# Kernel optimization log

Measured on AMD Instinct MI355X. Metric: run time of the kernel, lower is better.

## Reference

```python
import jax, jax.numpy as jnp
import numpy as np

B, GL, GF, N = 4, 4, 128, 1024
CS, CN, NA = 32, 16, 16
S, HS = 512, 512


def squash(s, axis):
    # mag_sq/(1+mag_sq) * s/mag == s * mag/(1+mag_sq)
    mag_sq = jnp.sum(s * s, axis=axis, keepdims=True)
    return s * (jnp.sqrt(mag_sq) / (1.0 + mag_sq))


def routing(u_hat, n_iter=3):
    # u_hat: [M, I, J, U]; dynamic routing, softmax over J, squash over J (as in source)
    M, I, J, U = u_hat.shape
    b = jnp.zeros((I, J), dtype=u_hat.dtype)
    v = None
    for _ in range(n_iter):
        c = jax.nn.softmax(b, axis=1)                       # [I, J]
        s = jnp.einsum('ij,miju->mju', c, u_hat)            # [M, J, U]
        v = squash(s, axis=1)                               # squash over J (torch dim=2)
        b = b + jnp.einsum('miju,mju->mij', u_hat, v).mean(axis=0)
    return v


def setup_inputs():
    key = jax.random.key(0)
    ks = jax.random.split(key, 7)
    sc = 0.1
    return {
        'graph_embed': jax.random.normal(ks[0], (B, GL, GF, N), jnp.float32),
        'hidden': jax.random.normal(ks[1], (B, S, HS), jnp.float32),
        'Wp': jax.random.normal(ks[2], (GL, CS, GL, GF), jnp.float32) * sc,  # per-unit conv kernels
        'bp': jax.random.normal(ks[3], (GL, CS), jnp.float32) * sc,
        'Wg': jax.random.normal(ks[4], (CS, CN, CS, GL), jnp.float32) * sc,  # graph caps [I,J,U,K]
        'Wa': jax.random.normal(ks[5], (CS + HS,), jnp.float32) * sc,        # attention_1 weight
        'Ws': jax.random.normal(ks[6], (CN, NA, CS, CS), jnp.float32) * sc,  # aspect caps [I,J,U,K]
    }


def _per_example(x, h, Wp, bp, Wg, Wa, Ws):
    # x: [GL, GF, N], h: [S, HS]
    gl, gf, n = x.shape
    # primary capsules: each unit's conv kernel covers all (GL,GF) -> full contraction
    u = jnp.einsum('uclf,lfn->ucn', Wp, x) + bp[:, :, None]   # [GL, CS, N]
    u = squash(u.reshape(gl, -1), axis=1)                     # squash over CS*N (torch dim=2)
    p = u.reshape(n, gl, CS)                                  # torch .view(-1, GL, CS)
    # graph capsule routing
    u_hat_g = jnp.einsum('ijuk,mik->miju', Wg, p.transpose(0, 2, 1))  # [N, CS, CN, CS]
    v_g = routing(u_hat_g)                                    # [N, CN, CS]
    g = v_g.reshape(n, CS, CN).mean(axis=0).reshape(CN, CS)   # torch .view semantics
    # adaptive attention: Linear([g;h]) with no bias, softmax over capsules
    score = jax.nn.softmax((g @ Wa[:CS])[None, :] + (h @ Wa[CS:])[:, None], axis=1)  # [S, CN]
    condensed = g[None, :, :] * score[:, :, None]             # [S, CN, CS]
    # aspect capsule routing (transpose(1,2) then layer-internal transpose cancel out)
    u_hat_a = jnp.einsum('ijuk,mik->miju', Ws, condensed)     # [S, CN, NA, CS]
    return routing(u_hat_a)                                   # [S, NA, CS]


def reference(graph_embed, hidden, Wp, bp, Wg, Wa, Ws):
    f = jax.vmap(_per_example, in_axes=(0, 0, None, None, None, None, None))
    return f(graph_embed, hidden, Wp, bp, Wg, Wa, Ws)   # [B, S, NA, CS]
```

## Files before the change

### kernel.cpp

```cpp
#include <hip/hip_runtime.h>
#include <math.h>


static constexpr int OFF_U  = 0;
static constexpr int OFF_S  = 524288;
static constexpr int OFF_SS = 2621440;
static constexpr int OFF_BG = 2621456;
static constexpr int OFF_G  = 2623504;
static constexpr int OFF_VA = 2625552;
static constexpr int OFF_MS = 2627600;
static constexpr int OFF_UH = 2758672;

__global__ void k_primary_part(const float* __restrict__ X, const float* __restrict__ Wp,
                               float* __restrict__ Upart)
{
    __shared__ float Wt[128 * 68];
    const int ct = blockIdx.x, nt = blockIdx.y;
    const int b = blockIdx.z >> 2, ks = blockIdx.z & 3;
    const int t = threadIdx.x;
    const int tn = t & 15, tc = t >> 4;
    const int c0 = ct * 64, n0 = nt * 64;
#pragma unroll
    for (int i = 0; i < 8; ++i) {
        const int idx = t + i * 256;
        const int c = idx >> 5, k4 = idx & 31;
        const float4 wv = *(const float4*)&Wp[(size_t)(c0 + c) * 512 + ks * 128 + k4 * 4];
        Wt[(k4 * 4 + 0) * 68 + c] = wv.x;
        Wt[(k4 * 4 + 1) * 68 + c] = wv.y;
        Wt[(k4 * 4 + 2) * 68 + c] = wv.z;
        Wt[(k4 * 4 + 3) * 68 + c] = wv.w;
    }
    __syncthreads();
    float acc[4][4] = {};
    const float* Xp = X + (size_t)b * 524288 + (size_t)(ks * 128) * 1024 + n0 + tn * 4;
#pragma unroll 4
    for (int k = 0; k < 128; ++k) {
        const float4 xv = *(const float4*)(Xp + (size_t)k * 1024);
        const float4 wv = *(const float4*)&Wt[k * 68 + tc * 4];
        const float w[4] = {wv.x, wv.y, wv.z, wv.w};
        const float x[4] = {xv.x, xv.y, xv.z, xv.w};
#pragma unroll
        for (int ci = 0; ci < 4; ++ci)
#pragma unroll
            for (int ni = 0; ni < 4; ++ni)
                acc[ci][ni] = fmaf(w[ci], x[ni], acc[ci][ni]);
    }
    float* up = Upart + (size_t)ks * 524288 + (size_t)b * 131072;
#pragma unroll
    for (int ci = 0; ci < 4; ++ci)
        *(float4*)&up[(size_t)(c0 + tc * 4 + ci) * 1024 + n0 + tn * 4] =
            make_float4(acc[ci][0], acc[ci][1], acc[ci][2], acc[ci][3]);
}

__global__ void k_reduceU(const float* __restrict__ Upart, const float* __restrict__ bp,
                          float* __restrict__ U, float* __restrict__ SS)
{
    __shared__ float red[256];
    const int blk = blockIdx.x, t = threadIdx.x;
    const int b = blk >> 5, cg = blk & 31;
    float ssq = 0.f;
#pragma unroll
    for (int i = 0; i < 4; ++i) {
        const int c = cg * 4 + i;
        const int f4 = b * 32768 + c * 256 + t;
        float4 s = ((const float4*)Upart)[f4];
#pragma unroll
        for (int ks = 1; ks < 4; ++ks) {
            const float4 p = ((const float4*)Upart)[ks * 131072 + f4];
            s.x += p.x; s.y += p.y; s.z += p.z; s.w += p.w;
        }
        const float bv = bp[c];
        s.x += bv; s.y += bv; s.z += bv; s.w += bv;
        ssq = fmaf(s.x, s.x, ssq); ssq = fmaf(s.y, s.y, ssq);
        ssq = fmaf(s.z, s.z, ssq); ssq = fmaf(s.w, s.w, ssq);
        ((float4*)U)[f4] = s;
    }
    red[t] = ssq;
    __syncthreads();
    for (int s = 128; s > 0; s >>= 1) {
        if (t < s) red[t] += red[t + s];
        __syncthreads();
    }
    if (t == 0) atomicAdd(&SS[b * 4 + (cg >> 3)], red[0]);
}

__global__ void k_smatmul(const float* __restrict__ U, const float* __restrict__ SS,
                          const float* __restrict__ Bg, const float* __restrict__ Wg,
                          float* __restrict__ S)
{
    __shared__ float Pt[64 * 65];
    __shared__ float Ct[64 * 65];
    __shared__ float cls[512];
    const int mt = blockIdx.x, jt = blockIdx.y, b = blockIdx.z;
    const int t = threadIdx.x;
    const int tj = t & 15, tm = t >> 4;
    if (t < 32) {
        float vals[16];
        float mx = -1e30f;
        for (int j = 0; j < 16; ++j) { vals[j] = Bg[b * 512 + t * 16 + j]; mx = fmaxf(mx, vals[j]); }
        float sum = 0.f;
        for (int j = 0; j < 16; ++j) { vals[j] = expf(vals[j] - mx); sum += vals[j]; }
        const float inv = 1.f / sum;
        for (int j = 0; j < 16; ++j) cls[t * 16 + j] = vals[j] * inv;
    }
    const float ss = SS[b * 4 + (mt >> 2)];
    const float sc = sqrtf(ss) / (1.f + ss);
    float acc[4][4] = {};
    const float* Ub = U + (size_t)b * 131072 + (size_t)mt * 64 * 128;
    __syncthreads();
    for (int kc = 0; kc < 2; ++kc) {
        for (int x = t; x < 64 * 64; x += 256) {
            const int r = x >> 6, cq = x & 63;
            Pt[r * 65 + cq] = Ub[r * 128 + kc * 64 + cq] * sc;
            const int q = kc * 64 + cq;
            const int i = q & 31, kk = q >> 5;
            const int ju = jt * 64 + r;
            const int j = ju >> 5, u = ju & 31;
            Ct[r * 65 + cq] = cls[i * 16 + j] * Wg[((i * 16 + j) * 32 + u) * 4 + kk];
        }
        __syncthreads();
        for (int q = 0; q < 64; ++q) {
            float pv[4], cv[4];
#pragma unroll
            for (int mm = 0; mm < 4; ++mm) pv[mm] = Pt[(tm * 4 + mm) * 65 + q];
#pragma unroll
            for (int jj = 0; jj < 4; ++jj) cv[jj] = Ct[(tj * 4 + jj) * 65 + q];
#pragma unroll
            for (int mm = 0; mm < 4; ++mm)
#pragma unroll
                for (int jj = 0; jj < 4; ++jj)
                    acc[mm][jj] = fmaf(pv[mm], cv[jj], acc[mm][jj]);
        }
        __syncthreads();
    }
#pragma unroll
    for (int mm = 0; mm < 4; ++mm) {
        float4 w = make_float4(acc[mm][0], acc[mm][1], acc[mm][2], acc[mm][3]);
        *(float4*)(S + (size_t)b * 524288 + (size_t)(mt * 64 + tm * 4 + mm) * 512
                     + jt * 64 + tj * 4) = w;
    }
}

__global__ void k_mag(const float* __restrict__ S, float* __restrict__ MS)
{
    const int t = threadIdx.x;
    const int u = t & 31, ml = t >> 5;
    const int m = blockIdx.x * 8 + ml;
    const int b = blockIdx.y;
    const float* row = S + (size_t)b * 524288 + (size_t)m * 512;
    float mag = 0.f;
#pragma unroll
    for (int j = 0; j < 16; ++j) { const float v = row[j * 32 + u]; mag = fmaf(v, v, mag); }
    MS[b * 32768 + m * 32 + u] = sqrtf(mag) / (1.f + mag);
}

__global__ void k_maggmean(const float* __restrict__ S, float* __restrict__ G)
{
    __shared__ float gacc[512];
    const int t = threadIdx.x;
    gacc[t] = 0.f; gacc[t + 256] = 0.f;
    const int u = t & 31, mlg = t >> 5;
    const int b = blockIdx.y;
    const int m0 = blockIdx.x * 32 + mlg * 4;
    float preg[16];
#pragma unroll
    for (int j = 0; j < 16; ++j) preg[j] = 0.f;
    __syncthreads();
#pragma unroll
    for (int mi = 0; mi < 4; ++mi) {
        const float* row = S + (size_t)b * 524288 + (size_t)(m0 + mi) * 512;
        float sv[16];
        float mag = 0.f;
#pragma unroll
        for (int j = 0; j < 16; ++j) { sv[j] = row[j * 32 + u]; mag = fmaf(sv[j], sv[j], mag); }
        const float msc = sqrtf(mag) / (1.f + mag);
#pragma unroll
        for (int j = 0; j < 16; ++j) preg[j] = fmaf(sv[j], msc, preg[j]);
    }
#pragma unroll
    for (int j = 0; j < 16; ++j) atomicAdd(&gacc[j * 32 + u], preg[j]);
    __syncthreads();
    atomicAdd(&G[b * 512 + t], gacc[t] * (1.f / 1024.f));
    atomicAdd(&G[b * 512 + 256 + t], gacc[t + 256] * (1.f / 1024.f));
}

__global__ void k_tbu(const float* __restrict__ U, const float* __restrict__ SS,
                      const float* __restrict__ S, const float* __restrict__ MS,
                      const float* __restrict__ Wg, float* __restrict__ Bg)
{
    __shared__ float Ps[64 * 132];
    __shared__ float Vs[64 * 68];
    __shared__ float bup[64];
    const int jt = blockIdx.x, mc = blockIdx.y, b = blockIdx.z;
    const int t = threadIdx.x;
    const int tq = t & 31, tjv = t >> 5;
    const int m0 = mc * 64;
    if (t < 64) bup[t] = 0.f;
    const float ss = SS[b * 4 + (mc >> 2)];
    const float sc = sqrtf(ss) / (1.f + ss);
#pragma unroll
    for (int i = 0; i < 8; ++i) {
        const int f4 = t + i * 256;
        const int r = f4 >> 5, q4 = f4 & 31;
        float4 v = *(const float4*)&U[(size_t)b * 131072 + (size_t)(m0 + r) * 128 + q4 * 4];
        v.x *= sc; v.y *= sc; v.z *= sc; v.w *= sc;
        *(float4*)&Ps[r * 132 + q4 * 4] = v;
    }
#pragma unroll
    for (int i = 0; i < 4; ++i) {
        const int f4 = t + i * 256;
        const int r = f4 >> 4, c4 = f4 & 15;
        const int m = m0 + r;
        float4 v = *(const float4*)&S[(size_t)b * 524288 + (size_t)m * 512 + jt * 64 + c4 * 4];
        const int ub = (c4 * 4) & 31;
        const float* msp = MS + b * 32768 + m * 32;
        v.x *= msp[ub + 0]; v.y *= msp[ub + 1]; v.z *= msp[ub + 2]; v.w *= msp[ub + 3];
        *(float4*)&Vs[r * 68 + c4 * 4] = v;
    }
    __syncthreads();
    float acc[4][8] = {};
#pragma unroll 2
    for (int m = 0; m < 64; ++m) {
        const float4 p4 = *(const float4*)&Ps[m * 132 + tq * 4];
        const float4 va = *(const float4*)&Vs[m * 68 + tjv * 8];
        const float4 vb = *(const float4*)&Vs[m * 68 + tjv * 8 + 4];
        const float pv[4] = {p4.x, p4.y, p4.z, p4.w};
        const float vv[8] = {va.x, va.y, va.z, va.w, vb.x, vb.y, vb.z, vb.w};
#pragma unroll
        for (int qi = 0; qi < 4; ++qi)
#pragma unroll
            for (int ji = 0; ji < 8; ++ji)
                acc[qi][ji] = fmaf(pv[qi], vv[ji], acc[qi][ji]);
    }
    const int k = tq >> 3;
    const int j_loc = tjv >> 2;
    const int j = jt * 2 + j_loc;
    const int u0 = (tjv & 3) * 8;
#pragma unroll
    for (int qi = 0; qi < 4; ++qi) {
        const int i = (tq & 7) * 4 + qi;
        const float* wp = Wg + ((i * 16 + j) * 32) * 4 + k;
        float s = 0.f;
#pragma unroll
        for (int ji = 0; ji < 8; ++ji)
            s = fmaf(wp[(u0 + ji) * 4], acc[qi][ji], s);
        s += __shfl_xor(s, 8);
        s += __shfl_xor(s, 16);
        s += __shfl_xor(s, 32);
        if ((t & 56) == 0) atomicAdd(&bup[i * 2 + j_loc], s);
    }
    __syncthreads();
    if (t < 64) {
        const int ii = t >> 1, jl = t & 1;
        atomicAdd(&Bg[b * 512 + ii * 16 + jt * 2 + jl], bup[t] * (1.f / 1024.f));
    }
}

__global__ void k_uhat(const float* __restrict__ G, const float* __restrict__ Wa,
                       const float* __restrict__ Ws, float* __restrict__ UH)
{
    const int b = blockIdx.y;
    const int t = threadIdx.x;
    __shared__ float g[512], cond[512], score[16], red[16];
    g[t] = G[b * 512 + t];
    g[t + 256] = G[b * 512 + 256 + t];
    __syncthreads();
    if (t < 16) {
        float s = 0.f;
        for (int u = 0; u < 32; ++u) s = fmaf(g[t * 32 + u], Wa[u], s);
        red[t] = s;
    }
    __syncthreads();
    if (t == 0) {
        float mx = -1e30f;
        for (int j = 0; j < 16; ++j) mx = fmaxf(mx, red[j]);
        float sum = 0.f;
        for (int j = 0; j < 16; ++j) { score[j] = expf(red[j] - mx); sum += score[j]; }
        const float inv = 1.f / sum;
        for (int j = 0; j < 16; ++j) score[j] *= inv;
    }
    __syncthreads();
    cond[t] = g[t] * score[t >> 5];
    cond[t + 256] = g[t + 256] * score[(t + 256) >> 5];
    __syncthreads();
    const int e0 = blockIdx.x * 1024 + t * 4;
    const int i = e0 >> 9;
    const float* cp = cond + i * 32;
    const float* wp = Ws + (size_t)e0 * 32;
    float res[4];
#pragma unroll
    for (int jj = 0; jj < 4; ++jj) {
        float s = 0.f;
#pragma unroll
        for (int k8 = 0; k8 < 8; ++k8) {
            const float4 w = *(const float4*)(wp + jj * 32 + k8 * 4);
            s = fmaf(w.x, cp[k8 * 4 + 0], s);
            s = fmaf(w.y, cp[k8 * 4 + 1], s);
            s = fmaf(w.z, cp[k8 * 4 + 2], s);
            s = fmaf(w.w, cp[k8 * 4 + 3], s);
        }
        res[jj] = s;
    }
    ((float4*)UH)[(b * 8192 + e0) >> 2] = make_float4(res[0], res[1], res[2], res[3]);
}

__global__ void k_route(const float* __restrict__ UH, float* __restrict__ VA)
{
    const int b = blockIdx.x;
    const int t = threadIdx.x;
    __shared__ float uh[8192], ba[256], cc[256], sbuf[512], msc[32];
#pragma unroll
    for (int i = 0; i < 8; ++i)
        ((float4*)uh)[i * 256 + t] = ((const float4*)UH)[b * 2048 + i * 256 + t];
    ba[t] = 0.f;
    __syncthreads();
    for (int it = 0; it < 3; ++it) {
        if (t < 16) {
            float mx = -1e30f;
            for (int j = 0; j < 16; ++j) mx = fmaxf(mx, ba[t * 16 + j]);
            float sum = 0.f;
            for (int j = 0; j < 16; ++j) { cc[t * 16 + j] = expf(ba[t * 16 + j] - mx); sum += cc[t * 16 + j]; }
            const float inv = 1.f / sum;
            for (int j = 0; j < 16; ++j) cc[t * 16 + j] *= inv;
        }
        __syncthreads();
        for (int h = 0; h < 2; ++h) {
            const int e = h * 256 + t;
            const int j = e >> 5;
            float s = 0.f;
            for (int i = 0; i < 16; ++i) s = fmaf(cc[i * 16 + j], uh[i * 512 + e], s);
            sbuf[e] = s;
        }
        __syncthreads();
        if (t < 32) {
            float mg = 0.f;
            for (int j = 0; j < 16; ++j) { const float x = sbuf[j * 32 + t]; mg = fmaf(x, x, mg); }
            msc[t] = sqrtf(mg) / (1.f + mg);
        }
        __syncthreads();
        for (int h = 0; h < 2; ++h) {
            const int e = h * 256 + t;
            sbuf[e] *= msc[e & 31];
        }
        __syncthreads();
        if (it < 2) {
            const int i = t >> 4, j = t & 15;
            float s = 0.f;
            for (int u = 0; u < 32; ++u) s = fmaf(uh[i * 512 + j * 32 + u], sbuf[j * 32 + u], s);
            ba[t] += s;
            __syncthreads();
        }
    }
    VA[b * 512 + t] = sbuf[t];
    VA[b * 512 + 256 + t] = sbuf[256 + t];
}

__global__ void k_out(const float* __restrict__ VA, float* __restrict__ out)
{
    const int idx = blockIdx.x * 256 + threadIdx.x;
    const int b = idx >> 16;
    const int jv4 = idx & 127;
    ((float4*)out)[idx] = ((const float4*)VA)[b * 128 + jv4];
}

extern "C" void kernel_launch(void* const* d_in, const int* in_sizes, int n_in,
                              void* d_out, int out_size, void* d_ws, size_t ws_size,
                              hipStream_t stream)
{
    const float* X   = (const float*)d_in[0];
    const float* Wp  = (const float*)d_in[2];
    const float* bp  = (const float*)d_in[3];
    const float* Wg  = (const float*)d_in[4];
    const float* Wa  = (const float*)d_in[5];
    const float* Wsp = (const float*)d_in[6];
    float* out = (float*)d_out;
    float* ws = (float*)d_ws;

    float* U  = ws + OFF_U;
    float* S  = ws + OFF_S;
    float* SS = ws + OFF_SS;
    float* Bg = ws + OFF_BG;
    float* G  = ws + OFF_G;
    float* VA = ws + OFF_VA;
    float* MS = ws + OFF_MS;
    float* UH = ws + OFF_UH;

    hipMemsetAsync(SS, 0, (16 + 2048 + 2048) * sizeof(float), stream);

    k_primary_part<<<dim3(2, 16, 16), 256, 0, stream>>>(X, Wp, S);
    k_reduceU<<<128, 256, 0, stream>>>(S, bp, U, SS);

    for (int it = 0; it < 3; ++it) {
        k_smatmul<<<dim3(16, 8, 4), 256, 0, stream>>>(U, SS, Bg, Wg, S);
        if (it < 2) {
            k_mag<<<dim3(128, 4), 256, 0, stream>>>(S, MS);
            k_tbu<<<dim3(8, 16, 4), 256, 0, stream>>>(U, SS, S, MS, Wg, Bg);
        } else {
            k_maggmean<<<dim3(32, 4), 256, 0, stream>>>(S, G);
        }
    }

    k_uhat<<<dim3(8, 4), 256, 0, stream>>>(G, Wa, Wsp, UH);
    k_route<<<4, 256, 0, stream>>>(UH, VA);
    k_out<<<1024, 256, 0, stream>>>(VA, out);
}
```

Before: 230.1 us.

## Fold memset, magnitude and output-broadcast kernels into neighbouring kernels

Removes the memset by zeroing the accumulators inside the first kernel, fuses the per-row squash-magnitude computation into the agreement kernel via shared memory, and merges routing with the output broadcast. The aim is to cut kernel launch count and the MS global buffer. In exchange, magnitudes are recomputed redundantly by each column-tile block and routing is redone in every output block.

```diff
diff --git a/kernel.cpp b/kernel.cpp
--- a/kernel.cpp
+++ b/kernel.cpp
@@ -7,14 +7,17 @@
 static constexpr int OFF_SS = 2621440;
 static constexpr int OFF_BG = 2621456;
 static constexpr int OFF_G  = 2623504;
-static constexpr int OFF_VA = 2625552;
-static constexpr int OFF_MS = 2627600;
-static constexpr int OFF_UH = 2758672;
+static constexpr int OFF_UH = 2625552;
 
 __global__ void k_primary_part(const float* __restrict__ X, const float* __restrict__ Wp,
-                               float* __restrict__ Upart)
+                               float* __restrict__ ws)
 {
     __shared__ float Wt[128 * 68];
+    float* Upart = ws + OFF_S;
+    if (blockIdx.x == 0 && blockIdx.y == 0 && blockIdx.z == 0) {
+        float* Z = ws + OFF_SS;
+        for (int i = threadIdx.x; i < 4112; i += 256) Z[i] = 0.f;
+    }
     const int ct = blockIdx.x, nt = blockIdx.y;
     const int b = blockIdx.z >> 2, ks = blockIdx.z & 3;
     const int t = threadIdx.x;
@@ -52,10 +55,12 @@
             make_float4(acc[ci][0], acc[ci][1], acc[ci][2], acc[ci][3]);
 }
 
-__global__ void k_reduceU(const float* __restrict__ Upart, const float* __restrict__ bp,
-                          float* __restrict__ U, float* __restrict__ SS)
+__global__ void k_reduceU(const float* __restrict__ bp, float* __restrict__ ws)
 {
     __shared__ float red[256];
+    const float* Upart = ws + OFF_S;
+    float* U  = ws + OFF_U;
+    float* SS = ws + OFF_SS;
     const int blk = blockIdx.x, t = threadIdx.x;
     const int b = blk >> 5, cg = blk & 31;
     float ssq = 0.f;
@@ -84,13 +89,15 @@
     if (t == 0) atomicAdd(&SS[b * 4 + (cg >> 3)], red[0]);
 }
 
-__global__ void k_smatmul(const float* __restrict__ U, const float* __restrict__ SS,
-                          const float* __restrict__ Bg, const float* __restrict__ Wg,
-                          float* __restrict__ S)
+__global__ void k_smatmul(const float* __restrict__ Wg, float* __restrict__ ws)
 {
     __shared__ float Pt[64 * 65];
     __shared__ float Ct[64 * 65];
     __shared__ float cls[512];
+    const float* U  = ws + OFF_U;
+    const float* SS = ws + OFF_SS;
+    const float* Bg = ws + OFF_BG;
+    float* S = ws + OFF_S;
     const int mt = blockIdx.x, jt = blockIdx.y, b = blockIdx.z;
     const int t = threadIdx.x;
     const int tj = t & 15, tm = t >> 4;
@@ -103,8 +110,8 @@
         const float inv = 1.f / sum;
         for (int j = 0; j < 16; ++j) cls[t * 16 + j] = vals[j] * inv;
     }
-    const float ss = SS[b * 4 + (mt >> 2)];
-    const float sc = sqrtf(ss) / (1.f + ss);
+    const float ssv = SS[b * 4 + (mt >> 2)];
+    const float sc = sqrtf(ssv) / (1.f + ssv);
     float acc[4][4] = {};
     const float* Ub = U + (size_t)b * 131072 + (size_t)mt * 64 * 128;
     __syncthreads();
@@ -115,8 +122,8 @@
             const int q = kc * 64 + cq;
             const int i = q & 31, kk = q >> 5;
             const int ju = jt * 64 + r;
-            const int j = ju >> 5, u = ju & 31;
-            Ct[r * 65 + cq] = cls[i * 16 + j] * Wg[((i * 16 + j) * 32 + u) * 4 + kk];
+            const int j = ju >> 5, uu = ju & 31;
+            Ct[r * 65 + cq] = cls[i * 16 + j] * Wg[((i * 16 + j) * 32 + uu) * 4 + kk];
         }
         __syncthreads();
         for (int q = 0; q < 64; ++q) {
@@ -141,63 +148,36 @@
     }
 }
 
-__global__ void k_mag(const float* __restrict__ S, float* __restrict__ MS)
-{
-    const int t = threadIdx.x;
-    const int u = t & 31, ml = t >> 5;
-    const int m = blockIdx.x * 8 + ml;
-    const int b = blockIdx.y;
-    const float* row = S + (size_t)b * 524288 + (size_t)m * 512;
-    float mag = 0.f;
-#pragma unroll
-    for (int j = 0; j < 16; ++j) { const float v = row[j * 32 + u]; mag = fmaf(v, v, mag); }
-    MS[b * 32768 + m * 32 + u] = sqrtf(mag) / (1.f + mag);
-}
-
-__global__ void k_maggmean(const float* __restrict__ S, float* __restrict__ G)
-{
-    __shared__ float gacc[512];
-    const int t = threadIdx.x;
-    gacc[t] = 0.f; gacc[t + 256] = 0.f;
-    const int u = t & 31, mlg = t >> 5;
-    const int b = blockIdx.y;
-    const int m0 = blockIdx.x * 32 + mlg * 4;
-    float preg[16];
-#pragma unroll
-    for (int j = 0; j < 16; ++j) preg[j] = 0.f;
-    __syncthreads();
-#pragma unroll
-    for (int mi = 0; mi < 4; ++mi) {
-        const float* row = S + (size_t)b * 524288 + (size_t)(m0 + mi) * 512;
-        float sv[16];
-        float mag = 0.f;
-#pragma unroll
-        for (int j = 0; j < 16; ++j) { sv[j] = row[j * 32 + u]; mag = fmaf(sv[j], sv[j], mag); }
-        const float msc = sqrtf(mag) / (1.f + mag);
-#pragma unroll
-        for (int j = 0; j < 16; ++j) preg[j] = fmaf(sv[j], msc, preg[j]);
-    }
-#pragma unroll
-    for (int j = 0; j < 16; ++j) atomicAdd(&gacc[j * 32 + u], preg[j]);
-    __syncthreads();
-    atomicAdd(&G[b * 512 + t], gacc[t] * (1.f / 1024.f));
-    atomicAdd(&G[b * 512 + 256 + t], gacc[t + 256] * (1.f / 1024.f));
-}
-
-__global__ void k_tbu(const float* __restrict__ U, const float* __restrict__ SS,
-                      const float* __restrict__ S, const float* __restrict__ MS,
-                      const float* __restrict__ Wg, float* __restrict__ Bg)
+__global__ void k_tbu(const float* __restrict__ Wg, float* __restrict__ ws)
 {
     __shared__ float Ps[64 * 132];
     __shared__ float Vs[64 * 68];
+    __shared__ float msS[64 * 32];
     __shared__ float bup[64];
+    const float* U  = ws + OFF_U;
+    const float* SS = ws + OFF_SS;
+    const float* S  = ws + OFF_S;
+    float* Bg = ws + OFF_BG;
     const int jt = blockIdx.x, mc = blockIdx.y, b = blockIdx.z;
     const int t = threadIdx.x;
     const int tq = t & 31, tjv = t >> 5;
     const int m0 = mc * 64;
     if (t < 64) bup[t] = 0.f;
-    const float ss = SS[b * 4 + (mc >> 2)];
-    const float sc = sqrtf(ss) / (1.f + ss);
+    {
+        const int uu = t & 31, rg = t >> 5;
+#pragma unroll
+        for (int mi = 0; mi < 8; ++mi) {
+            const int r = rg * 8 + mi;
+            const float* row = S + (size_t)b * 524288 + (size_t)(m0 + r) * 512;
+            float mag = 0.f;
+#pragma unroll
+            for (int j = 0; j < 16; ++j) { const float v = row[j * 32 + uu]; mag = fmaf(v, v, mag); }
+            msS[r * 32 + uu] = sqrtf(mag) / (1.f + mag);
+        }
+    }
+    const float ssv = SS[b * 4 + (mc >> 2)];
+    const float sc = sqrtf(ssv) / (1.f + ssv);
+    __syncthreads();
 #pragma unroll
     for (int i = 0; i < 8; ++i) {
         const int f4 = t + i * 256;
@@ -213,8 +193,8 @@
         const int m = m0 + r;
         float4 v = *(const float4*)&S[(size_t)b * 524288 + (size_t)m * 512 + jt * 64 + c4 * 4];
         const int ub = (c4 * 4) & 31;
-        const float* msp = MS + b * 32768 + m * 32;
-        v.x *= msp[ub + 0]; v.y *= msp[ub + 1]; v.z *= msp[ub + 2]; v.w *= msp[ub + 3];
+        v.x *= msS[r * 32 + ub + 0]; v.y *= msS[r * 32 + ub + 1];
+        v.z *= msS[r * 32 + ub + 2]; v.w *= msS[r * 32 + ub + 3];
         *(float4*)&Vs[r * 68 + c4 * 4] = v;
     }
     __syncthreads();
@@ -256,9 +236,43 @@
     }
 }
 
-__global__ void k_uhat(const float* __restrict__ G, const float* __restrict__ Wa,
-                       const float* __restrict__ Ws, float* __restrict__ UH)
-{
+__global__ void k_maggmean(float* __restrict__ ws)
+{
+    __shared__ float gacc[512];
+    const float* S = ws + OFF_S;
+    float* G = ws + OFF_G;
+    const int t = threadIdx.x;
+    gacc[t] = 0.f; gacc[t + 256] = 0.f;
+    const int uu = t & 31, mlg = t >> 5;
+    const int b = blockIdx.y;
+    const int m0 = blockIdx.x * 32 + mlg * 4;
+    float preg[16];
+#pragma unroll
+    for (int j = 0; j < 16; ++j) preg[j] = 0.f;
+    __syncthreads();
+#pragma unroll
+    for (int mi = 0; mi < 4; ++mi) {
+        const float* row = S + (size_t)b * 524288 + (size_t)(m0 + mi) * 512;
+        float sv[16];
+        float mag = 0.f;
+#pragma unroll
+        for (int j = 0; j < 16; ++j) { sv[j] = row[j * 32 + uu]; mag = fmaf(sv[j], sv[j], mag); }
+        const float msc = sqrtf(mag) / (1.f + mag);
+#pragma unroll
+        for (int j = 0; j < 16; ++j) preg[j] = fmaf(sv[j], msc, preg[j]);
+    }
+#pragma unroll
+    for (int j = 0; j < 16; ++j) atomicAdd(&gacc[j * 32 + uu], preg[j]);
+    __syncthreads();
+    atomicAdd(&G[b * 512 + t], gacc[t] * (1.f / 1024.f));
+    atomicAdd(&G[b * 512 + 256 + t], gacc[t + 256] * (1.f / 1024.f));
+}
+
+__global__ void k_uhat(const float* __restrict__ Wa, const float* __restrict__ Wsp,
+                       float* __restrict__ ws)
+{
+    const float* G = ws + OFF_G;
+    float* UH = ws + OFF_UH;
     const int b = blockIdx.y;
     const int t = threadIdx.x;
     __shared__ float g[512], cond[512], score[16], red[16];
@@ -267,7 +281,7 @@
     __syncthreads();
     if (t < 16) {
         float s = 0.f;
-        for (int u = 0; u < 32; ++u) s = fmaf(g[t * 32 + u], Wa[u], s);
+        for (int uu = 0; uu < 32; ++uu) s = fmaf(g[t * 32 + uu], Wa[uu], s);
         red[t] = s;
     }
     __syncthreads();
@@ -286,7 +300,7 @@
     const int e0 = blockIdx.x * 1024 + t * 4;
     const int i = e0 >> 9;
     const float* cp = cond + i * 32;
-    const float* wp = Ws + (size_t)e0 * 32;
+    const float* wp = Wsp + (size_t)e0 * 32;
     float res[4];
 #pragma unroll
     for (int jj = 0; jj < 4; ++jj) {
@@ -304,11 +318,13 @@
     ((float4*)UH)[(b * 8192 + e0) >> 2] = make_float4(res[0], res[1], res[2], res[3]);
 }
 
-__global__ void k_route(const float* __restrict__ UH, float* __restrict__ VA)
-{
-    const int b = blockIdx.x;
+__global__ void k_route_out(float* __restrict__ ws, float* __restrict__ out)
+{
+    const float* UH = ws + OFF_UH;
+    const int bid = blockIdx.x;
     const int t = threadIdx.x;
     __shared__ float uh[8192], ba[256], cc[256], sbuf[512], msc[32];
+    const int b = bid >> 6;
 #pragma unroll
     for (int i = 0; i < 8; ++i)
         ((float4*)uh)[i * 256 + t] = ((const float4*)UH)[b * 2048 + i * 256 + t];
@@ -346,21 +362,17 @@
         if (it < 2) {
             const int i = t >> 4, j = t & 15;
             float s = 0.f;
-            for (int u = 0; u < 32; ++u) s = fmaf(uh[i * 512 + j * 32 + u], sbuf[j * 32 + u], s);
+            for (int uu = 0; uu < 32; ++uu) s = fmaf(uh[i * 512 + j * 32 + uu], sbuf[j * 32 + uu], s);
             ba[t] += s;
             __syncthreads();
         }
     }
-    VA[b * 512 + t] = sbuf[t];
-    VA[b * 512 + 256 + t] = sbuf[256 + t];
-}
-
-__global__ void k_out(const float* __restrict__ VA, float* __restrict__ out)
-{
-    const int idx = blockIdx.x * 256 + threadIdx.x;
-    const int b = idx >> 16;
-    const int jv4 = idx & 127;
-    ((float4*)out)[idx] = ((const float4*)VA)[b * 128 + jv4];
+#pragma unroll
+    for (int i = 0; i < 4; ++i) {
+        const int idx = bid * 1024 + i * 256 + t;
+        const int jv4 = idx & 127;
+        ((float4*)out)[idx] = *(const float4*)&sbuf[jv4 * 4];
+    }
 }
 
 extern "C" void kernel_launch(void* const* d_in, const int* in_sizes, int n_in,
@@ -374,33 +386,17 @@
     const float* Wa  = (const float*)d_in[5];
     const float* Wsp = (const float*)d_in[6];
     float* out = (float*)d_out;
-    float* ws = (float*)d_ws;
-
-    float* U  = ws + OFF_U;
-    float* S  = ws + OFF_S;
-    float* SS = ws + OFF_SS;
-    float* Bg = ws + OFF_BG;
-    float* G  = ws + OFF_G;
-    float* VA = ws + OFF_VA;
-    float* MS = ws + OFF_MS;
-    float* UH = ws + OFF_UH;
-
-    hipMemsetAsync(SS, 0, (16 + 2048 + 2048) * sizeof(float), stream);
-
-    k_primary_part<<<dim3(2, 16, 16), 256, 0, stream>>>(X, Wp, S);
-    k_reduceU<<<128, 256, 0, stream>>>(S, bp, U, SS);
+    float* ws  = (float*)d_ws;
+
+    k_primary_part<<<dim3(2, 16, 16), 256, 0, stream>>>(X, Wp, ws);
+    k_reduceU<<<128, 256, 0, stream>>>(bp, ws);
 
     for (int it = 0; it < 3; ++it) {
-        k_smatmul<<<dim3(16, 8, 4), 256, 0, stream>>>(U, SS, Bg, Wg, S);
-        if (it < 2) {
-            k_mag<<<dim3(128, 4), 256, 0, stream>>>(S, MS);
-            k_tbu<<<dim3(8, 16, 4), 256, 0, stream>>>(U, SS, S, MS, Wg, Bg);
-        } else {
-            k_maggmean<<<dim3(32, 4), 256, 0, stream>>>(S, G);
-        }
-    }
-
-    k_uhat<<<dim3(8, 4), 256, 0, stream>>>(G, Wa, Wsp, UH);
-    k_route<<<4, 256, 0, stream>>>(UH, VA);
-    k_out<<<1024, 256, 0, stream>>>(VA, out);
-}
+        k_smatmul<<<dim3(16, 8, 4), 256, 0, stream>>>(Wg, ws);
+        if (it < 2) k_tbu<<<dim3(8, 16, 4), 256, 0, stream>>>(Wg, ws);
+        else        k_maggmean<<<dim3(32, 4), 256, 0, stream>>>(ws);
+    }
+
+    k_uhat<<<dim3(8, 4), 256, 0, stream>>>(Wa, Wsp, ws);
+    k_route_out<<<256, 256, 0, stream>>>(ws, out);
+}
```

New measurement: 231.6 us. Within noise of the previous version (+0.7%).
